# Kernel optimization log

Hardware: AMD Instinct MI355X
Metric: run time of the kernel (lower is better)

Reference implementation:

```python
import jax, jax.numpy as jnp
import numpy as np

NUM_HEADS = 8

def dwconv(x, w, b, pad):
    # depthwise conv: x [B, C, H, W], w [C, 1, k, k], groups=C
    y = jax.lax.conv_general_dilated(
        x, w, window_strides=(1, 1), padding=[(pad, pad), (pad, pad)],
        feature_group_count=x.shape[1], dimension_numbers=('NCHW', 'OIHW', 'NCHW'))
    return y + b[None, :, None, None]


def setup_inputs() -> dict:
    key = jax.random.key(0)
    ks = jax.random.split(key, 12)
    B, H, W = 32, 28, 28
    C = 512
    N = 1 + H * W
    Ch = C // NUM_HEADS  # 64
    s = lambda k, shp, fan: jax.random.normal(k, shp, jnp.float32) * (fan ** -0.5)
    return {
        'x': jax.random.normal(ks[0], (B, N, C), jnp.float32),
        'qkv_w': s(ks[1], (3 * C, C), C),
        'qkv_b': jnp.zeros((3 * C,), jnp.float32),
        'proj_w': s(ks[2], (C, C), C),
        'proj_b': jnp.zeros((C,), jnp.float32),
        'w3': s(ks[3], (2 * Ch, 1, 3, 3), 9),
        'b3': jnp.zeros((2 * Ch,), jnp.float32),
        'w5': s(ks[4], (3 * Ch, 1, 5, 5), 25),
        'b5': jnp.zeros((3 * Ch,), jnp.float32),
        'w7': s(ks[5], (3 * Ch, 1, 7, 7), 49),
        'b7': jnp.zeros((3 * Ch,), jnp.float32),
        'H': H,
        'W': W,
    }


def reference(x, qkv_w, qkv_b, proj_w, proj_b, w3, b3, w5, b5, w7, b7, H, W):
    B, N, C = x.shape
    h = NUM_HEADS
    Ch = C // h
    scale = Ch ** -0.5
    # qkv projection -> q, k, v each [B, h, N, Ch]
    qkv = (x @ qkv_w.T + qkv_b).reshape(B, N, 3, h, Ch).transpose(2, 0, 3, 1, 4)
    q, k, v = qkv[0], qkv[1], qkv[2]
    # factorized attention: softmax over tokens on k, then (k^T v) then q @ ...
    k_sm = jax.nn.softmax(k, axis=2)
    kv = jnp.einsum('bhnc,bhnd->bhcd', k_sm, v)          # [B,h,Ch,Ch]
    factor_att = jnp.einsum('bhnc,bhcd->bhnd', q, kv)    # [B,h,N,Ch]
    # conv relative position encoding (CRPE) on image tokens only
    q_img = q[:, :, 1:, :]                               # [B,h,HW,Ch]
    v_img = v[:, :, 1:, :].transpose(0, 1, 3, 2).reshape(B, h * Ch, H, W)
    splits = np.cumsum([2 * Ch, 3 * Ch, 3 * Ch])[:-1]
    v1, v2, v3 = jnp.split(v_img, splits, axis=1)
    conv_v = jnp.concatenate(
        [dwconv(v1, w3, b3, 1), dwconv(v2, w5, b5, 2), dwconv(v3, w7, b7, 3)], axis=1)
    conv_v = conv_v.reshape(B, h, Ch, H * W).transpose(0, 1, 3, 2)  # [B,h,HW,Ch]
    EV = q_img * conv_v
    crpe = jnp.pad(EV, ((0, 0), (0, 0), (1, 0), (0, 0)))  # zero row for cls token
    out = scale * factor_att + crpe
    out = out.transpose(0, 2, 1, 3).reshape(B, N, C)
    return out @ proj_w.T + proj_b
```

## Files before the change

### kernel.cpp

```cpp
#include <hip/hip_runtime.h>
#include <cstdint>
#include <cstddef>


typedef unsigned short u16;

#define HEADS 8
#define CHD   64
#define CDIM  512
#define NTOK  785
#define BATCH 32
#define MROWS (BATCH * NTOK)
#define MPAD  25344
#define QKVN  1536
#define IMGHW 784
#define KVSPLIT 7

typedef float  f32x4  __attribute__((ext_vector_type(4)));
typedef __bf16 bf16x8 __attribute__((ext_vector_type(8)));

__device__ __forceinline__ u16 f2bf(float f) {
  union { float f; uint32_t u; } x; x.f = f;
  uint32_t r = x.u + 0x7fffu + ((x.u >> 16) & 1u);
  return (u16)(r >> 16);
}
__device__ __forceinline__ float bf2f(u16 u) {
  union { uint32_t u; float f; } x; x.u = ((uint32_t)u) << 16;
  return x.f;
}
__device__ __forceinline__ uint32_t pk2(float a, float b) {
#if __has_builtin(__builtin_amdgcn_cvt_pk_bf16_f32)
  auto v = __builtin_amdgcn_cvt_pk_bf16_f32(a, b);
  union { decltype(v) v2; uint32_t u; } cv; cv.v2 = v; return cv.u;
#else
  return (uint32_t)f2bf(a) | ((uint32_t)f2bf(b) << 16);
#endif
}

__global__ __launch_bounds__(256)
void casts_kernel(const float* __restrict__ x, u16* __restrict__ xb,
                  const float* __restrict__ w1, u16* __restrict__ w1b,
                  const float* __restrict__ w2, u16* __restrict__ w2b) {
  const int N1 = MROWS * CDIM / 4, N2 = QKVN * CDIM / 4, N3 = CDIM * CDIM / 4;
  int i = blockIdx.x * 256 + threadIdx.x;
  const float* src; u16* dst;
  if (i < N1)           { src = x;  dst = xb;  }
  else if (i < N1 + N2) { i -= N1;  src = w1; dst = w1b; }
  else if (i < N1 + N2 + N3) { i -= N1 + N2; src = w2; dst = w2b; }
  else return;
  float4 v = reinterpret_cast<const float4*>(src)[i];
  uint2 o; o.x = pk2(v.x, v.y); o.y = pk2(v.z, v.w);
  reinterpret_cast<uint2*>(dst)[i] = o;
}

__device__ __forceinline__ void gld_lds16(const u16* g, u16* l) {
  __builtin_amdgcn_global_load_lds((__attribute__((address_space(1))) void*)g,
                                   (__attribute__((address_space(3))) void*)l,
                                   16, 0, 0);
}

template <int OUTBF16>
__global__ __launch_bounds__(512)
void gemm_bt(const u16* __restrict__ A, const u16* __restrict__ W,
             const float* __restrict__ bias, void* __restrict__ Cout,
             int Mstore, int N, int K, int nMt, int nNt) {
  __shared__ __align__(16) u16 lsA[256 * 64];
  __shared__ __align__(16) u16 lsB[128 * 64];
  const int flat = blockIdx.x;
  const int xcd = flat & 7, idx = flat >> 3;
  const int nt = idx % nNt;
  const int mt = (idx / nNt) * 8 + xcd;
  if (mt >= nMt) return;
  const int tile_m = mt * 256, tile_n = nt * 128;

  const int tid  = threadIdx.x;
  const int wave = tid >> 6, lane = tid & 63;
  const int quad = lane >> 4, l16 = lane & 15;
  const int wm = (wave & 3) * 64, wn = (wave >> 2) * 64;

  const int srow0 = tid >> 3;
  const int scol  = ((tid & 7) ^ (srow0 & 7)) * 8;
  const int ldst  = srow0 * 64 + (tid & 7) * 8;

  f32x4 acc[4][4] = {};

  for (int k0 = 0; k0 < K; k0 += 64) {
#pragma unroll
    for (int s = 0; s < 4; ++s)
      gld_lds16(A + (size_t)(tile_m + s * 64 + srow0) * K + k0 + scol,
                &lsA[s * 4096 + ldst]);
#pragma unroll
    for (int s = 0; s < 2; ++s)
      gld_lds16(W + (size_t)(tile_n + s * 64 + srow0) * K + k0 + scol,
                &lsB[s * 4096 + ldst]);
    __syncthreads();
#pragma unroll
    for (int kk = 0; kk < 2; ++kk) {
      const int pch = ((kk * 4 + quad) ^ (l16 & 7)) * 8;
      bf16x8 af[4], bfr[4];
#pragma unroll
      for (int i = 0; i < 4; ++i) {
        af[i]  = *reinterpret_cast<const bf16x8*>(&lsA[(wm + i * 16 + l16) * 64 + pch]);
        bfr[i] = *reinterpret_cast<const bf16x8*>(&lsB[(wn + i * 16 + l16) * 64 + pch]);
      }
#pragma unroll
      for (int i = 0; i < 4; ++i)
#pragma unroll
        for (int j = 0; j < 4; ++j)
          acc[i][j] = __builtin_amdgcn_mfma_f32_16x16x32_bf16(af[i], bfr[j], acc[i][j], 0, 0, 0);
    }
    __syncthreads();
  }

#pragma unroll
  for (int i = 0; i < 4; ++i) {
    const int mbase = tile_m + wm + i * 16 + quad * 4;
#pragma unroll
    for (int j = 0; j < 4; ++j) {
      const int n  = tile_n + wn + j * 16 + l16;
      const float bv = bias[n];
      const float v0 = acc[i][j][0] + bv, v1 = acc[i][j][1] + bv;
      const float v2 = acc[i][j][2] + bv, v3 = acc[i][j][3] + bv;
      if (OUTBF16) {
        u16* cp = reinterpret_cast<u16*>(Cout) + (size_t)mbase * N + n;
        const uint32_t p01 = pk2(v0, v1), p23 = pk2(v2, v3);
        if (mbase + 0 < Mstore) cp[0]            = (u16)p01;
        if (mbase + 1 < Mstore) cp[(size_t)N]    = (u16)(p01 >> 16);
        if (mbase + 2 < Mstore) cp[(size_t)N*2]  = (u16)p23;
        if (mbase + 3 < Mstore) cp[(size_t)N*3]  = (u16)(p23 >> 16);
      } else {
        float* cp = reinterpret_cast<float*>(Cout) + (size_t)mbase * N + n;
        if (mbase + 0 < Mstore) cp[0]           = v0;
        if (mbase + 1 < Mstore) cp[(size_t)N]   = v1;
        if (mbase + 2 < Mstore) cp[(size_t)N*2] = v2;
        if (mbase + 3 < Mstore) cp[(size_t)N*3] = v3;
      }
    }
  }
}

__global__ __launch_bounds__(256)
void kv_kernel(const u16* __restrict__ qkv, float* __restrict__ kvpart,
               float* __restrict__ kvsum) {
  const int bh = blockIdx.x, split = blockIdx.y;
  const int b = bh >> 3, h = bh & 7;
  const int n_start = split * 113;
  const int n_end = min(NTOK, n_start + 113);
  const int t = threadIdx.x;
  const int d = t & 63, cq = t >> 6;
  __shared__ float e_s[32 * 64];
  __shared__ float v_s[32 * 64];
  const u16* kbase = qkv + (size_t)(b * NTOK) * QKVN + CDIM + h * CHD;
  const u16* vbase = kbase + CDIM;
  float acc[16];
#pragma unroll
  for (int i = 0; i < 16; ++i) acc[i] = 0.f;
  float s_part = 0.f;

  for (int n0 = n_start; n0 < n_end; n0 += 32) {
    const int nc = min(32, n_end - n0);
    __syncthreads();
    for (int i = t; i < nc * 64; i += 256) {
      const int nl = i >> 6, c = i & 63;
      const float e = __expf(bf2f(kbase[(size_t)(n0 + nl) * QKVN + c]));
      e_s[i] = e; s_part += e;
      v_s[i] = bf2f(vbase[(size_t)(n0 + nl) * QKVN + c]);
    }
    __syncthreads();
    for (int nl = 0; nl < nc; ++nl) {
      const float vv = v_s[nl * 64 + d];
#pragma unroll
      for (int i = 0; i < 16; ++i)
        acc[i] += e_s[nl * 64 + cq * 16 + i] * vv;
    }
  }
#pragma unroll
  for (int i = 0; i < 16; ++i) {
    const int c = cq * 16 + i;
    kvpart[(((size_t)bh * KVSPLIT + split) * 64 + c) * 64 + d] = acc[i];
  }
  __syncthreads();
  e_s[t] = s_part;
  __syncthreads();
  if (t < 64)
    kvsum[((size_t)bh * KVSPLIT + split) * 64 + t] =
        e_s[t] + e_s[64 + t] + e_s[128 + t] + e_s[192 + t];
}

__global__ __launch_bounds__(256)
void kv_reduce_kernel(const float* __restrict__ kvpart, const float* __restrict__ kvsum,
                      u16* __restrict__ kvT) {
  const int bh = blockIdx.x;
  const int t = threadIdx.x;
  const int d = t & 63, cq = t >> 6;
#pragma unroll
  for (int cc = 0; cc < 16; ++cc) {
    const int c = cq * 16 + cc;
    float s = 0.f, S = 0.f;
#pragma unroll
    for (int sp = 0; sp < KVSPLIT; ++sp) {
      s += kvpart[(((size_t)bh * KVSPLIT + sp) * 64 + c) * 64 + d];
      S += kvsum[((size_t)bh * KVSPLIT + sp) * 64 + c];
    }
    kvT[(size_t)bh * 4096 + d * 64 + c] = f2bf(s / S);
  }
}

template <int KS>
__device__ __forceinline__ void conv_head(
    const u16* __restrict__ qkv, const float* __restrict__ wgt,
    const float* __restrict__ bias, int b, int head, int hh, int yt,
    u16* __restrict__ evbuf, u16* __restrict__ ls) {
  constexpr int PAD = KS / 2;
  constexpr int RIN = 4 + 2 * PAD;
  const int t = threadIdx.x;
  const int y0 = yt * 4;
  const u16* vimg = qkv + (size_t)(b * NTOK + 1) * QKVN + 2 * CDIM + head * 64;
  const int c8 = (t & 7) * 8;
  for (int pi = t >> 3; pi < RIN * 28; pi += 32) {
    const int ry = pi / 28, rx = pi - ry * 28;
    const int yy = y0 - PAD + ry;
    uint4 val = {0, 0, 0, 0};
    if (yy >= 0 && yy < 28)
      val = *reinterpret_cast<const uint4*>(vimg + (size_t)(yy * 28 + rx) * QKVN + c8);
    *reinterpret_cast<uint4*>(ls + pi * 64 + c8) = val;
  }
  __syncthreads();
  const int d = t & 63, yl = t >> 6;
  float wr[KS * KS];
  const float* wp = wgt + (hh * 64 + d) * KS * KS;
#pragma unroll
  for (int i = 0; i < KS * KS; ++i) wr[i] = wp[i];
  const float bv = bias[hh * 64 + d];
  float acc[28];
#pragma unroll
  for (int x = 0; x < 28; ++x) acc[x] = bv;
#pragma unroll
  for (int xx = 0; xx < 28; ++xx) {
    float col[KS];
#pragma unroll
    for (int r = 0; r < KS; ++r)
      col[r] = bf2f(ls[((yl + r) * 28 + xx) * 64 + d]);
#pragma unroll
    for (int j = 0; j < KS; ++j) {
      const int x = xx + PAD - j;
      if (x >= 0 && x < 28) {
#pragma unroll
        for (int r = 0; r < KS; ++r)
          acc[x] += col[r] * wr[r * KS + j];
      }
    }
  }
  const int p0 = (y0 + yl) * 28;
  const u16* qrow = qkv + (size_t)(b * NTOK + 1 + p0) * QKVN + head * 64 + d;
  u16* obase = evbuf + (((size_t)(b * 8 + head)) * IMGHW + p0) * 64 + d;
#pragma unroll
  for (int x = 0; x < 28; ++x) {
    const float ev = acc[x] * bf2f(qrow[(size_t)x * QKVN]);
    obase[(size_t)x * 64] = f2bf(ev);
  }
}

__global__ __launch_bounds__(256)
void conv_all_kernel(const u16* __restrict__ qkv,
                     const float* __restrict__ w3, const float* __restrict__ b3,
                     const float* __restrict__ w5, const float* __restrict__ b5,
                     const float* __restrict__ w7, const float* __restrict__ b7,
                     u16* __restrict__ evbuf) {
  __shared__ __align__(16) u16 ls[10 * 28 * 64];
  const int b = blockIdx.x, h = blockIdx.y, yt = blockIdx.z;
  if (h < 2)      conv_head<3>(qkv, w3, b3, b, h, h,     yt, evbuf, ls);
  else if (h < 5) conv_head<5>(qkv, w5, b5, b, h, h - 2, yt, evbuf, ls);
  else            conv_head<7>(qkv, w7, b7, b, h, h - 5, yt, evbuf, ls);
}

__global__ __launch_bounds__(256)
void combine_kernel(const u16* __restrict__ qkv, const u16* __restrict__ kvT,
                    const u16* __restrict__ evbuf, u16* __restrict__ attn) {
  const int bh = blockIdx.x;
  const int b = bh >> 3, h = bh & 7;
  const int wave = threadIdx.x >> 6, lane = threadIdx.x & 63;
  const int quad = lane >> 4, l16 = lane & 15;
  const int tokbase = blockIdx.y * 256 + wave * 64;

  const u16* kvb = kvT + (size_t)bh * 4096;
  bf16x8 bfr[4][2];
#pragma unroll
  for (int j = 0; j < 4; ++j)
#pragma unroll
    for (int kk = 0; kk < 2; ++kk)
      bfr[j][kk] = *reinterpret_cast<const bf16x8*>(
          &kvb[(j * 16 + l16) * 64 + kk * 32 + quad * 8]);

  bf16x8 af[4][2];
#pragma unroll
  for (int i = 0; i < 4; ++i) {
    const int tok = min(tokbase + i * 16 + l16, NTOK - 1);
    const u16* qrow = qkv + (size_t)(b * NTOK + tok) * QKVN + h * CHD;
    af[i][0] = *reinterpret_cast<const bf16x8*>(&qrow[quad * 8]);
    af[i][1] = *reinterpret_cast<const bf16x8*>(&qrow[32 + quad * 8]);
  }

  f32x4 acc[4][4] = {};
#pragma unroll
  for (int kk = 0; kk < 2; ++kk)
#pragma unroll
    for (int i = 0; i < 4; ++i)
#pragma unroll
      for (int j = 0; j < 4; ++j)
        acc[i][j] = __builtin_amdgcn_mfma_f32_16x16x32_bf16(af[i][kk], bfr[j][kk], acc[i][j], 0, 0, 0);

  const float scale = 0.125f;
  const u16* evb = evbuf + (size_t)bh * IMGHW * 64;
#pragma unroll
  for (int i = 0; i < 4; ++i) {
#pragma unroll
    for (int r = 0; r < 4; ++r) {
      const int tok = tokbase + i * 16 + quad * 4 + r;
      if (tok < NTOK) {
#pragma unroll
        for (int j = 0; j < 4; ++j) {
          const int d = j * 16 + l16;
          float out = scale * acc[i][j][r];
          if (tok > 0) out += bf2f(evb[(size_t)(tok - 1) * 64 + d]);
          attn[(size_t)(b * NTOK + tok) * CDIM + h * CHD + d] = f2bf(out);
        }
      }
    }
  }
}

extern "C" void kernel_launch(void* const* d_in, const int* in_sizes, int n_in,
                              void* d_out, int out_size, void* d_ws, size_t ws_size,
                              hipStream_t stream) {
  const float* x      = (const float*)d_in[0];
  const float* qkv_w  = (const float*)d_in[1];
  const float* qkv_b  = (const float*)d_in[2];
  const float* proj_w = (const float*)d_in[3];
  const float* proj_b = (const float*)d_in[4];
  const float* w3 = (const float*)d_in[5];
  const float* b3 = (const float*)d_in[6];
  const float* w5 = (const float*)d_in[7];
  const float* b5 = (const float*)d_in[8];
  const float* w7 = (const float*)d_in[9];
  const float* b7 = (const float*)d_in[10];
  float* out = (float*)d_out;

  char* p = (char*)d_ws;
  u16* xb    = (u16*)p;   p += (size_t)MPAD * CDIM * 2;
  u16* wqb   = (u16*)p;   p += (size_t)QKVN * CDIM * 2;
  u16* wpb   = (u16*)p;   p += (size_t)CDIM * CDIM * 2;
  u16* qkvb  = (u16*)p;   p += (size_t)MPAD * QKVN * 2;
  float* kvsum = (float*)p; p += (size_t)256 * KVSPLIT * 64 * 4;
  u16* kvT   = (u16*)p;   p += (size_t)256 * 64 * 64 * 2;
  char* shared_region = p;
  float* kvpart = (float*)shared_region;
  u16*   evbuf  = (u16*)shared_region;
  p += (size_t)256 * KVSPLIT * 64 * 64 * 4;
  u16* attn  = (u16*)p;   p += (size_t)MPAD * CDIM * 2;

  {
    const int total = MROWS * CDIM / 4 + QKVN * CDIM / 4 + CDIM * CDIM / 4;
    casts_kernel<<<(total + 255) / 256, 256, 0, stream>>>(x, xb, qkv_w, wqb, proj_w, wpb);
  }
  gemm_bt<1><<<13 * 8 * 12, 512, 0, stream>>>(xb, wqb, qkv_b, qkvb,
                                              MPAD, QKVN, CDIM, 99, 12);
  kv_kernel<<<dim3(256, KVSPLIT), 256, 0, stream>>>(qkvb, kvpart, kvsum);
  kv_reduce_kernel<<<256, 256, 0, stream>>>(kvpart, kvsum, kvT);
  conv_all_kernel<<<dim3(BATCH, HEADS, 7), 256, 0, stream>>>(
      qkvb, w3, b3, w5, b5, w7, b7, evbuf);
  combine_kernel<<<dim3(256, 4), 256, 0, stream>>>(qkvb, kvT, evbuf, attn);
  gemm_bt<0><<<13 * 8 * 4, 512, 0, stream>>>(attn, wpb, proj_b, out,
                                             MROWS, CDIM, CDIM, 99, 4);
}
```

Before: 326.0 us.

## Double-buffer LDS tiles in bf16 GEMM to overlap global loads with MFMA

Adds a second LDS buffer for the A and B tiles in the GEMM. The next K-slice is prefetched via global_load_lds while MFMAs run on the current buffer, which should hide global memory latency. s_setprio is also raised around the MFMA block. LDS use doubles to 96KB per block, which may cut occupancy. The loop relies on a single barrier per iteration to cover the async LDS loads; that synchronisation is delicate, since global_load_lds completion depends on vmcnt waits that the barrier may insert.

After: 355.6 us. 9.1% more time.

```diff
diff --git a/kernel.cpp b/kernel.cpp
--- a/kernel.cpp
+++ b/kernel.cpp
@@ -64,8 +64,8 @@
 void gemm_bt(const u16* __restrict__ A, const u16* __restrict__ W,
              const float* __restrict__ bias, void* __restrict__ Cout,
              int Mstore, int N, int K, int nMt, int nNt) {
-  __shared__ __align__(16) u16 lsA[256 * 64];
-  __shared__ __align__(16) u16 lsB[128 * 64];
+  __shared__ __align__(16) u16 lsA[2][256 * 64];
+  __shared__ __align__(16) u16 lsB[2][128 * 64];
   const int flat = blockIdx.x;
   const int xcd = flat & 7, idx = flat >> 3;
   const int nt = idx % nNt;
@@ -84,32 +84,48 @@
 
   f32x4 acc[4][4] = {};
 
+#pragma unroll
+  for (int s = 0; s < 4; ++s)
+    gld_lds16(A + (size_t)(tile_m + s * 64 + srow0) * K + scol,
+              &lsA[0][s * 4096 + ldst]);
+#pragma unroll
+  for (int s = 0; s < 2; ++s)
+    gld_lds16(W + (size_t)(tile_n + s * 64 + srow0) * K + scol,
+              &lsB[0][s * 4096 + ldst]);
+  __syncthreads();
+
+  int cur = 0;
   for (int k0 = 0; k0 < K; k0 += 64) {
-#pragma unroll
-    for (int s = 0; s < 4; ++s)
-      gld_lds16(A + (size_t)(tile_m + s * 64 + srow0) * K + k0 + scol,
-                &lsA[s * 4096 + ldst]);
-#pragma unroll
-    for (int s = 0; s < 2; ++s)
-      gld_lds16(W + (size_t)(tile_n + s * 64 + srow0) * K + k0 + scol,
-                &lsB[s * 4096 + ldst]);
-    __syncthreads();
+    if (k0 + 64 < K) {
+      const int kn = k0 + 64;
+#pragma unroll
+      for (int s = 0; s < 4; ++s)
+        gld_lds16(A + (size_t)(tile_m + s * 64 + srow0) * K + kn + scol,
+                  &lsA[cur ^ 1][s * 4096 + ldst]);
+#pragma unroll
+      for (int s = 0; s < 2; ++s)
+        gld_lds16(W + (size_t)(tile_n + s * 64 + srow0) * K + kn + scol,
+                  &lsB[cur ^ 1][s * 4096 + ldst]);
+    }
 #pragma unroll
     for (int kk = 0; kk < 2; ++kk) {
       const int pch = ((kk * 4 + quad) ^ (l16 & 7)) * 8;
       bf16x8 af[4], bfr[4];
 #pragma unroll
       for (int i = 0; i < 4; ++i) {
-        af[i]  = *reinterpret_cast<const bf16x8*>(&lsA[(wm + i * 16 + l16) * 64 + pch]);
-        bfr[i] = *reinterpret_cast<const bf16x8*>(&lsB[(wn + i * 16 + l16) * 64 + pch]);
+        af[i]  = *reinterpret_cast<const bf16x8*>(&lsA[cur][(wm + i * 16 + l16) * 64 + pch]);
+        bfr[i] = *reinterpret_cast<const bf16x8*>(&lsB[cur][(wn + i * 16 + l16) * 64 + pch]);
       }
+      __builtin_amdgcn_s_setprio(1);
 #pragma unroll
       for (int i = 0; i < 4; ++i)
 #pragma unroll
         for (int j = 0; j < 4; ++j)
           acc[i][j] = __builtin_amdgcn_mfma_f32_16x16x32_bf16(af[i], bfr[j], acc[i][j], 0, 0, 0);
+      __builtin_amdgcn_s_setprio(0);
     }
     __syncthreads();
+    cur ^= 1;
   }
 
 #pragma unroll
```

## Double-buffer LDS in bf16 GEMM with prefetch two K-tiles ahead

Applied to the files above, without the earlier changes.

Restructures the bf16 GEMM main loop to use two LDS buffers. The global-to-LDS loads for tile t+2 are issued while tile t is computed, with explicit vmcnt/lgkmcnt waits and raw s_barrier in place of __syncthreads. The loop is fully unrolled with a hardcoded 8 K-tiles (K=512), and MFMA sections get raised wave priority. The aim is to hide global load latency behind MFMA work, at the cost of doubled LDS use (lower occupancy) and a kernel that only supports K=512.

Measured after the change: 344.1 us. +5.5%, slower.

```diff
diff --git a/kernel.cpp b/kernel.cpp
--- a/kernel.cpp
+++ b/kernel.cpp
@@ -64,8 +64,9 @@
 void gemm_bt(const u16* __restrict__ A, const u16* __restrict__ W,
              const float* __restrict__ bias, void* __restrict__ Cout,
              int Mstore, int N, int K, int nMt, int nNt) {
-  __shared__ __align__(16) u16 lsA[256 * 64];
-  __shared__ __align__(16) u16 lsB[128 * 64];
+  constexpr int KT = 8;
+  __shared__ __align__(16) u16 lsA[2][256 * 64];
+  __shared__ __align__(16) u16 lsB[2][128 * 64];
   const int flat = blockIdx.x;
   const int xcd = flat & 7, idx = flat >> 3;
   const int nt = idx % nNt;
@@ -82,34 +83,70 @@
   const int scol  = ((tid & 7) ^ (srow0 & 7)) * 8;
   const int ldst  = srow0 * 64 + (tid & 7) * 8;
 
+  auto stage = [&](int kt, int buf) {
+    const int kc = kt * 64 + scol;
+#pragma unroll
+    for (int s = 0; s < 4; ++s)
+      gld_lds16(A + (size_t)(tile_m + s * 64 + srow0) * K + kc,
+                &lsA[buf][s * 4096 + ldst]);
+#pragma unroll
+    for (int s = 0; s < 2; ++s)
+      gld_lds16(W + (size_t)(tile_n + s * 64 + srow0) * K + kc,
+                &lsB[buf][s * 4096 + ldst]);
+  };
+
   f32x4 acc[4][4] = {};
 
-  for (int k0 = 0; k0 < K; k0 += 64) {
-#pragma unroll
-    for (int s = 0; s < 4; ++s)
-      gld_lds16(A + (size_t)(tile_m + s * 64 + srow0) * K + k0 + scol,
-                &lsA[s * 4096 + ldst]);
-#pragma unroll
-    for (int s = 0; s < 2; ++s)
-      gld_lds16(W + (size_t)(tile_n + s * 64 + srow0) * K + k0 + scol,
-                &lsB[s * 4096 + ldst]);
-    __syncthreads();
+  stage(0, 0);
+  stage(1, 1);
+  asm volatile("s_waitcnt vmcnt(6)" ::: "memory");
+  __builtin_amdgcn_sched_barrier(0);
+  __builtin_amdgcn_s_barrier();
+  __builtin_amdgcn_sched_barrier(0);
+
+#pragma unroll
+  for (int t = 0; t < KT; ++t) {
+    const int cur = t & 1;
+    bf16x8 af[2][4], bfr[2][4];
 #pragma unroll
     for (int kk = 0; kk < 2; ++kk) {
       const int pch = ((kk * 4 + quad) ^ (l16 & 7)) * 8;
-      bf16x8 af[4], bfr[4];
 #pragma unroll
       for (int i = 0; i < 4; ++i) {
-        af[i]  = *reinterpret_cast<const bf16x8*>(&lsA[(wm + i * 16 + l16) * 64 + pch]);
-        bfr[i] = *reinterpret_cast<const bf16x8*>(&lsB[(wn + i * 16 + l16) * 64 + pch]);
+        af[kk][i]  = *reinterpret_cast<const bf16x8*>(
+            &lsA[cur][(wm + i * 16 + l16) * 64 + pch]);
+        bfr[kk][i] = *reinterpret_cast<const bf16x8*>(
+            &lsB[cur][(wn + i * 16 + l16) * 64 + pch]);
       }
-#pragma unroll
-      for (int i = 0; i < 4; ++i)
-#pragma unroll
-        for (int j = 0; j < 4; ++j)
-          acc[i][j] = __builtin_amdgcn_mfma_f32_16x16x32_bf16(af[i], bfr[j], acc[i][j], 0, 0, 0);
-    }
-    __syncthreads();
+    }
+    __builtin_amdgcn_s_setprio(1);
+#pragma unroll
+    for (int i = 0; i < 4; ++i)
+#pragma unroll
+      for (int j = 0; j < 4; ++j)
+        acc[i][j] = __builtin_amdgcn_mfma_f32_16x16x32_bf16(
+            af[0][i], bfr[0][j], acc[i][j], 0, 0, 0);
+    __builtin_amdgcn_s_setprio(0);
+    asm volatile("s_waitcnt lgkmcnt(0)" ::: "memory");
+    __builtin_amdgcn_sched_barrier(0);
+    __builtin_amdgcn_s_barrier();
+    __builtin_amdgcn_sched_barrier(0);
+    if (t + 2 < KT) stage(t + 2, cur);
+    __builtin_amdgcn_s_setprio(1);
+#pragma unroll
+    for (int i = 0; i < 4; ++i)
+#pragma unroll
+      for (int j = 0; j < 4; ++j)
+        acc[i][j] = __builtin_amdgcn_mfma_f32_16x16x32_bf16(
+            af[1][i], bfr[1][j], acc[i][j], 0, 0, 0);
+    __builtin_amdgcn_s_setprio(0);
+    if (t + 1 < KT) {
+      if (t + 2 < KT) asm volatile("s_waitcnt vmcnt(6)" ::: "memory");
+      else            asm volatile("s_waitcnt vmcnt(0)" ::: "memory");
+      __builtin_amdgcn_sched_barrier(0);
+      __builtin_amdgcn_s_barrier();
+      __builtin_amdgcn_sched_barrier(0);
+    }
   }
 
 #pragma unroll
```

## Double-buffer GEMM LDS tiles with K-step 32 to overlap loads and MFMA

Applied to the files above, without the earlier changes.

Restructures the bf16 GEMM main loop to use two LDS buffers of K-width 32 instead of one of width 64. The next tile is issued via global_load_lds while the current one is consumed by MFMAs, removing one barrier per iteration and hiding global-load latency. The trade-off is half as much MFMA work per barrier, a new swizzle pattern for the narrower rows, and a correctness question about whether the async LDS loads finish before the single barrier that ends each iteration.

Result: no change. 327.3 us (+0.4%).

```diff
diff --git a/kernel.cpp b/kernel.cpp
--- a/kernel.cpp
+++ b/kernel.cpp
@@ -64,8 +64,8 @@
 void gemm_bt(const u16* __restrict__ A, const u16* __restrict__ W,
              const float* __restrict__ bias, void* __restrict__ Cout,
              int Mstore, int N, int K, int nMt, int nNt) {
-  __shared__ __align__(16) u16 lsA[256 * 64];
-  __shared__ __align__(16) u16 lsB[128 * 64];
+  __shared__ __align__(16) u16 lsA[2][256 * 32];
+  __shared__ __align__(16) u16 lsB[2][128 * 32];
   const int flat = blockIdx.x;
   const int xcd = flat & 7, idx = flat >> 3;
   const int nt = idx % nNt;
@@ -78,37 +78,44 @@
   const int quad = lane >> 4, l16 = lane & 15;
   const int wm = (wave & 3) * 64, wn = (wave >> 2) * 64;
 
-  const int srow0 = tid >> 3;
-  const int scol  = ((tid & 7) ^ (srow0 & 7)) * 8;
-  const int ldst  = srow0 * 64 + (tid & 7) * 8;
+  const int srow = tid >> 2;
+  const int scol = ((tid & 3) ^ ((tid >> 3) & 3)) * 8;
+  const int ldst = tid * 8;
+
+  auto stage = [&](int kt, int buf) {
+    const int kc = kt * 32 + scol;
+#pragma unroll
+    for (int s = 0; s < 2; ++s)
+      gld_lds16(A + (size_t)(tile_m + s * 128 + srow) * K + kc,
+                &lsA[buf][s * 4096 + ldst]);
+    gld_lds16(W + (size_t)(tile_n + srow) * K + kc, &lsB[buf][ldst]);
+  };
 
   f32x4 acc[4][4] = {};
 
-  for (int k0 = 0; k0 < K; k0 += 64) {
-#pragma unroll
-    for (int s = 0; s < 4; ++s)
-      gld_lds16(A + (size_t)(tile_m + s * 64 + srow0) * K + k0 + scol,
-                &lsA[s * 4096 + ldst]);
-#pragma unroll
-    for (int s = 0; s < 2; ++s)
-      gld_lds16(W + (size_t)(tile_n + s * 64 + srow0) * K + k0 + scol,
-                &lsB[s * 4096 + ldst]);
-    __syncthreads();
-#pragma unroll
-    for (int kk = 0; kk < 2; ++kk) {
-      const int pch = ((kk * 4 + quad) ^ (l16 & 7)) * 8;
-      bf16x8 af[4], bfr[4];
-#pragma unroll
-      for (int i = 0; i < 4; ++i) {
-        af[i]  = *reinterpret_cast<const bf16x8*>(&lsA[(wm + i * 16 + l16) * 64 + pch]);
-        bfr[i] = *reinterpret_cast<const bf16x8*>(&lsB[(wn + i * 16 + l16) * 64 + pch]);
-      }
-#pragma unroll
-      for (int i = 0; i < 4; ++i)
-#pragma unroll
-        for (int j = 0; j < 4; ++j)
-          acc[i][j] = __builtin_amdgcn_mfma_f32_16x16x32_bf16(af[i], bfr[j], acc[i][j], 0, 0, 0);
-    }
+  stage(0, 0);
+  __syncthreads();
+
+  const int KT = K >> 5;
+  const int pch = (quad ^ ((l16 >> 1) & 3)) * 8;
+#pragma unroll 2
+  for (int t = 0; t < KT; ++t) {
+    const int cur = t & 1;
+    if (t + 1 < KT) stage(t + 1, cur ^ 1);
+    bf16x8 af[4], bfr[4];
+#pragma unroll
+    for (int i = 0; i < 4; ++i) {
+      af[i]  = *reinterpret_cast<const bf16x8*>(
+          &lsA[cur][(wm + i * 16 + l16) * 32 + pch]);
+      bfr[i] = *reinterpret_cast<const bf16x8*>(
+          &lsB[cur][(wn + i * 16 + l16) * 32 + pch]);
+    }
+#pragma unroll
+    for (int i = 0; i < 4; ++i)
+#pragma unroll
+      for (int j = 0; j < 4; ++j)
+        acc[i][j] = __builtin_amdgcn_mfma_f32_16x16x32_bf16(
+            af[i], bfr[j], acc[i][j], 0, 0, 0);
     __syncthreads();
   }
 
```
